# Kernel optimization log

Hardware: AMD Instinct MI355X
Metric: run time of the kernel (lower is better)

The kernel has to match this reference:

```python
import jax, jax.numpy as jnp
import numpy as np

N_NODES = 50000
N_EDGES = 200000
NODE_F = 64
EDGE_F = 16
HID = 32
LAT = 16


def _glorot(key, shape):
    fan_in, fan_out = shape[0], shape[1]
    lim = np.sqrt(6.0 / (fan_in + fan_out))
    return jax.random.uniform(key, shape, jnp.float32, -lim, lim)


def setup_inputs() -> dict:
    key = jax.random.key(0)
    ks = jax.random.split(key, 24)
    inp = {
        "x": jax.random.normal(ks[0], (N_NODES, NODE_F), jnp.float32),
        "edge_index": jax.random.randint(ks[1], (2, N_EDGES), 0, N_NODES, jnp.int64),
        "edge_attr": jax.random.normal(ks[2], (N_EDGES, EDGE_F), jnp.float32),
        # encoder input projection
        "lin_in_w": _glorot(ks[3], (NODE_F, HID)),
        "lin_in_b": jnp.zeros((HID,), jnp.float32),
        # 3 edge MLPs (stacked over layer axis)
        "edge_w1": jnp.stack([_glorot(ks[4 + i], (EDGE_F, HID)) for i in range(3)]),
        "edge_b1": jnp.zeros((3, HID), jnp.float32),
        "edge_w2": jnp.stack([_glorot(ks[7 + i], (HID, HID * HID)) * 0.1 for i in range(3)]),
        "edge_b2": jnp.zeros((3, HID * HID), jnp.float32),
        # 3 NNConv root weights + biases
        "root_w": jnp.stack([_glorot(ks[10 + i], (HID, HID)) for i in range(3)]),
        "root_b": jnp.zeros((3, HID), jnp.float32),
        # encoder output projection
        "lin_out_w": _glorot(ks[13], (HID, LAT)),
        "lin_out_b": jnp.zeros((LAT,), jnp.float32),
        # node decoder MLP
        "dec_w1": _glorot(ks[14], (LAT, HID)),
        "dec_b1": jnp.zeros((HID,), jnp.float32),
        "dec_w2": _glorot(ks[15], (HID, NODE_F)),
        "dec_b2": jnp.zeros((NODE_F,), jnp.float32),
    }
    return inp


def _nnconv(x, src, dst, edge_attr, w1, b1, w2, b2, root_w, root_b):
    # per-edge weight matrix from edge MLP: [E, H, H]
    h = jax.nn.relu(edge_attr @ w1 + b1)
    w_e = (h @ w2 + b2).reshape(-1, HID, HID)
    # gather source features, per-edge matmul: [E, H]
    msg = jnp.einsum("eh,eho->eo", x[src], w_e)
    # scatter-mean to destinations
    agg = jax.ops.segment_sum(msg, dst, num_segments=N_NODES)
    cnt = jax.ops.segment_sum(jnp.ones((msg.shape[0], 1), x.dtype), dst, num_segments=N_NODES)
    agg = agg / jnp.maximum(cnt, 1.0)
    # root weight + bias
    return agg + x @ root_w + root_b


def reference(x, edge_index, edge_attr, lin_in_w, lin_in_b, edge_w1, edge_b1,
              edge_w2, edge_b2, root_w, root_b, lin_out_w, lin_out_b,
              dec_w1, dec_b1, dec_w2, dec_b2):
    src, dst = edge_index[0], edge_index[1]
    h = jax.nn.relu(x @ lin_in_w + lin_in_b)
    for i in range(3):  # fixed number of conv layers (dropout is identity in eval)
        h = _nnconv(h, src, dst, edge_attr, edge_w1[i], edge_b1[i],
                    edge_w2[i], edge_b2[i], root_w[i], root_b[i])
        h = jax.nn.relu(h)
    z = h @ lin_out_w + lin_out_b
    # node decoder
    d = jax.nn.relu(z @ dec_w1 + dec_b1)
    return d @ dec_w2 + dec_b2
```

## Files before the change

kernel.cpp:

```cpp
#include <hip/hip_runtime.h>
#include <hip/hip_bf16.h>
#include <stdint.h>

#define N_NODES 50000
#define N_EDGES 200000
#define NODE_F 64
#define EDGE_F 16
#define HID 32
#define LAT 16
#define KTOT 1056
#define SCAN_BLOCKS 196

typedef __attribute__((ext_vector_type(8))) short short8;
typedef __attribute__((ext_vector_type(4))) float f32x4;
typedef __attribute__((ext_vector_type(2))) float f32x2;

static __device__ __forceinline__ unsigned short bfbits(float f) {
  union { __hip_bfloat16 h; unsigned short s; } c; c.h = __float2bfloat16(f); return c.s;
}
static __device__ __forceinline__ unsigned pk2(f32x2 v) {
  __hip_bfloat162 h = __float22bfloat162_rn(make_float2(v.x, v.y));
  unsigned u; __builtin_memcpy(&u, &h, 4); return u;
}
static __device__ __forceinline__ unsigned pkt(f32x2 v) {
  return __builtin_amdgcn_perm(__float_as_uint(v.y), __float_as_uint(v.x), 0x07060302u);
}
union AFrag { short8 v; unsigned u[4]; };

__global__ void k_prep(const float* __restrict__ ew2, const float* __restrict__ eb2,
                       const float* __restrict__ ew1,
                       unsigned short* __restrict__ w2t,
                       unsigned short* __restrict__ w1p,
                       int* __restrict__ deg) {
  int g = blockIdx.x*256 + threadIdx.x;
  int l = g / (HID*KTOT);
  int r = g % (HID*KTOT);
  int o = r / KTOT;
  int kg = r % KTOT;
  int k = kg >> 5, h = kg & 31;
  float v = (k < 32) ? ew2[(size_t)l*32768 + k*1024 + h*32 + o]
                     : eb2[(size_t)l*1024 + h*32 + o];
  w2t[g] = bfbits(v);
  if (g < N_NODES) deg[g] = 0;
  if (g < 3*2*64*8) {
    int l2 = g >> 10;
    int r2 = g & 1023;
    int nt = r2 >> 9;
    int ln = (r2 >> 3) & 63;
    int j  = r2 & 7;
    int kgr = ln >> 4;
    float w = (kgr < 2) ? ew1[(size_t)l2*512 + (kgr*8 + j)*32 + nt*16 + (ln & 15)] : 0.f;
    w1p[g] = bfbits(w);
  }
}

__global__ void k_hist(const int* __restrict__ ei, int* __restrict__ deg) {
  int t = blockIdx.x*256 + threadIdx.x;
  if (t >= N_EDGES) return;
  int d = ei[N_EDGES + t];
  d = min(max(d, 0), N_NODES-1);
  atomicAdd(&deg[d], 1);
}

__global__ __launch_bounds__(256) void k_scan1(const int* __restrict__ deg,
                                               int* __restrict__ off,
                                               int* __restrict__ bsum) {
  __shared__ int s[256];
  const int tid = threadIdx.x;
  const int t = blockIdx.x*256 + tid;
  int d = (t < N_NODES) ? deg[t] : 0;
  s[tid] = d; __syncthreads();
  int v = d;
  #pragma unroll
  for (int ofs = 1; ofs < 256; ofs <<= 1) {
    int w = (tid >= ofs) ? s[tid-ofs] : 0;
    __syncthreads();
    v += w; s[tid] = v;
    __syncthreads();
  }
  if (t < N_NODES) off[t] = v - d;
  if (tid == 255) bsum[blockIdx.x] = v;
}

__global__ __launch_bounds__(256) void k_scan2(int* __restrict__ bsum) {
  __shared__ int s[256];
  const int tid = threadIdx.x;
  int d = (tid < SCAN_BLOCKS) ? bsum[tid] : 0;
  s[tid] = d; __syncthreads();
  int v = d;
  #pragma unroll
  for (int ofs = 1; ofs < 256; ofs <<= 1) {
    int w = (tid >= ofs) ? s[tid-ofs] : 0;
    __syncthreads();
    v += w; s[tid] = v;
    __syncthreads();
  }
  if (tid < SCAN_BLOCKS) bsum[tid] = v - d;
}

__global__ void k_scan3(int* __restrict__ off, const int* __restrict__ bsum,
                        int* __restrict__ cursor) {
  int t = blockIdx.x*256 + threadIdx.x;
  if (t < N_NODES) {
    off[t] += bsum[t >> 8];
    cursor[t] = 0;
  }
  if (t == 0) off[N_NODES] = N_EDGES;
}

__global__ void k_scatter(const int* __restrict__ ei, const int* __restrict__ off,
                          int* __restrict__ cursor, int* __restrict__ elist) {
  int t = blockIdx.x*256 + threadIdx.x;
  if (t >= N_EDGES) return;
  int d = ei[N_EDGES + t];
  d = min(max(d, 0), N_NODES-1);
  int pos = atomicAdd(&cursor[d], 1);
  elist[off[d] + pos] = t;
}

__global__ void k_lin_in(const float* __restrict__ x,
                         const float* __restrict__ W,
                         const float* __restrict__ b,
                         float* __restrict__ h) {
  __shared__ float Ws[NODE_F*HID];
  __shared__ float bs[HID];
  for (int i = threadIdx.x; i < NODE_F*HID; i += 256) Ws[i] = W[i];
  if (threadIdx.x < HID) bs[threadIdx.x] = b[threadIdx.x];
  __syncthreads();
  int t = blockIdx.x*256 + threadIdx.x;
  if (t >= N_NODES*HID) return;
  int n = t >> 5, o = t & 31;
  const float4* xp = (const float4*)(x + (size_t)n*NODE_F);
  float acc = bs[o];
  #pragma unroll
  for (int j = 0; j < NODE_F/4; j++) {
    float4 v = xp[j];
    acc = fmaf(v.x, Ws[(4*j+0)*HID+o], acc);
    acc = fmaf(v.y, Ws[(4*j+1)*HID+o], acc);
    acc = fmaf(v.z, Ws[(4*j+2)*HID+o], acc);
    acc = fmaf(v.w, Ws[(4*j+3)*HID+o], acc);
  }
  h[t] = fmaxf(acc, 0.f);
}

__global__ __launch_bounds__(256) void k_msg(const float* __restrict__ hin,
                                             const float* __restrict__ ea,
                                             const int* __restrict__ ei,
                                             const unsigned short* __restrict__ w1pl,
                                             const float* __restrict__ b1,
                                             const unsigned short* __restrict__ w2tl,
                                             float* __restrict__ msg) {
  __shared__ float sHE[128*33];
  __shared__ int   sSRC[128];
  const int tid = threadIdx.x;
  const int be  = blockIdx.x*128;
  const int wv   = tid >> 6;
  const int lane = tid & 63;
  const int nn   = lane & 15;
  const int quad = lane >> 4;
  const int eb0  = wv*32;
  const int eb1  = wv*32 + 16;

  if (lane < 32) {
    int e = min(be + wv*32 + lane, N_EDGES-1);
    sSRC[wv*32 + lane] = min(max(ei[e], 0), N_NODES-1);
    sHE[(wv*32 + lane)*33 + 32] = 1.0f;
  }

  {
    AFrag a0, a1;
    if (quad < 2) {
      int e0 = min(be + eb0 + nn, N_EDGES-1);
      int e1 = min(be + eb1 + nn, N_EDGES-1);
      const float4* p0 = (const float4*)(ea + (size_t)e0*EDGE_F + quad*8);
      const float4* p1 = (const float4*)(ea + (size_t)e1*EDGE_F + quad*8);
      float4 u = p0[0], v = p0[1];
      float4 s = p1[0], t = p1[1];
      a0.u[0] = pkt(f32x2{u.x,u.y}); a0.u[1] = pkt(f32x2{u.z,u.w});
      a0.u[2] = pkt(f32x2{v.x,v.y}); a0.u[3] = pkt(f32x2{v.z,v.w});
      a1.u[0] = pkt(f32x2{s.x,s.y}); a1.u[1] = pkt(f32x2{s.z,s.w});
      a1.u[2] = pkt(f32x2{t.x,t.y}); a1.u[3] = pkt(f32x2{t.z,t.w});
    } else {
      #pragma unroll
      for (int i = 0; i < 4; i++) { a0.u[i] = 0u; a1.u[i] = 0u; }
    }
    short8 wb0 = *(const short8*)(w1pl + lane*8);
    short8 wb1 = *(const short8*)(w1pl + 512 + lane*8);
    f32x4 z = {0.f,0.f,0.f,0.f};
    f32x4 h00 = __builtin_amdgcn_mfma_f32_16x16x32_bf16(a0.v, wb0, z, 0, 0, 0);
    f32x4 h01 = __builtin_amdgcn_mfma_f32_16x16x32_bf16(a0.v, wb1, z, 0, 0, 0);
    f32x4 h10 = __builtin_amdgcn_mfma_f32_16x16x32_bf16(a1.v, wb0, z, 0, 0, 0);
    f32x4 h11 = __builtin_amdgcn_mfma_f32_16x16x32_bf16(a1.v, wb1, z, 0, 0, 0);
    float bv0 = b1[nn], bv1 = b1[nn + 16];
    #pragma unroll
    for (int r = 0; r < 4; r++) {
      int ro0 = (eb0 + quad*4 + r)*33;
      int ro1 = (eb1 + quad*4 + r)*33;
      sHE[ro0 + nn]      = fmaxf(h00[r] + bv0, 0.f);
      sHE[ro0 + 16 + nn] = fmaxf(h01[r] + bv1, 0.f);
      sHE[ro1 + nn]      = fmaxf(h10[r] + bv0, 0.f);
      sHE[ro1 + 16 + nn] = fmaxf(h11[r] + bv1, 0.f);
    }
  }

  f32x2 xA[4], xB[4];
  {
    int s0i = sSRC[eb0+nn];
    int s1i = sSRC[eb1+nn];
    const float4* p0 = (const float4*)(hin + (size_t)s0i*HID);
    const float4* p1 = (const float4*)(hin + (size_t)s1i*HID);
    float4 a0 = p0[quad*2], a1 = p0[quad*2+1];
    float4 b0 = p1[quad*2], b1v = p1[quad*2+1];
    xA[0] = f32x2{a0.x, a0.y}; xA[1] = f32x2{a0.z, a0.w};
    xA[2] = f32x2{a1.x, a1.y}; xA[3] = f32x2{a1.z, a1.w};
    xB[0] = f32x2{b0.x, b0.y}; xB[1] = f32x2{b0.z, b0.w};
    xB[2] = f32x2{b1v.x, b1v.y}; xB[3] = f32x2{b1v.z, b1v.w};
  }

  f32x4 c00 = {0.f,0.f,0.f,0.f}, c01 = c00, c10 = c00, c11 = c00;
  const unsigned short* bp0 = w2tl + (unsigned)nn*KTOT + quad*8;
  const unsigned short* bp1 = bp0 + 16*KTOT;
  const float* heRow0 = sHE + (eb0+nn)*33;
  const float* heRow1 = sHE + (eb1+nn)*33;

  short8 sb0[3], sb1[3];
  float  sh0[3], sh1[3];
  #pragma unroll
  for (int j = 0; j < 3; j++) {
    sb0[j] = *(const short8*)(bp0 + j*32);
    sb1[j] = *(const short8*)(bp1 + j*32);
    sh0[j] = heRow0[j];
    sh1[j] = heRow1[j];
  }

  #pragma unroll 1
  for (int base = 0; base < 30; base += 3) {
    #pragma unroll
    for (int j = 0; j < 3; j++) {
      const int kk = base + j;
      float hk0 = sh0[j], hk1 = sh1[j];
      AFrag a0, a1;
      #pragma unroll
      for (int i = 0; i < 4; i++) {
        a0.u[i] = pkt(xA[i]*hk0);
        a1.u[i] = pkt(xB[i]*hk1);
      }
      short8 cb0 = sb0[j], cb1 = sb1[j];
      c00 = __builtin_amdgcn_mfma_f32_16x16x32_bf16(a0.v, cb0, c00, 0, 0, 0);
      c01 = __builtin_amdgcn_mfma_f32_16x16x32_bf16(a0.v, cb1, c01, 0, 0, 0);
      c10 = __builtin_amdgcn_mfma_f32_16x16x32_bf16(a1.v, cb0, c10, 0, 0, 0);
      c11 = __builtin_amdgcn_mfma_f32_16x16x32_bf16(a1.v, cb1, c11, 0, 0, 0);
      sb0[j] = *(const short8*)(bp0 + (kk+3)*32);
      sb1[j] = *(const short8*)(bp1 + (kk+3)*32);
      sh0[j] = heRow0[kk+3];
      sh1[j] = heRow1[kk+3];
    }
  }
  #pragma unroll
  for (int j = 0; j < 3; j++) {
    float hk0 = sh0[j], hk1 = sh1[j];
    AFrag a0, a1;
    #pragma unroll
    for (int i = 0; i < 4; i++) {
      a0.u[i] = pkt(xA[i]*hk0);
      a1.u[i] = pkt(xB[i]*hk1);
    }
    c00 = __builtin_amdgcn_mfma_f32_16x16x32_bf16(a0.v, sb0[j], c00, 0, 0, 0);
    c01 = __builtin_amdgcn_mfma_f32_16x16x32_bf16(a0.v, sb1[j], c01, 0, 0, 0);
    c10 = __builtin_amdgcn_mfma_f32_16x16x32_bf16(a1.v, sb0[j], c10, 0, 0, 0);
    c11 = __builtin_amdgcn_mfma_f32_16x16x32_bf16(a1.v, sb1[j], c11, 0, 0, 0);
  }

  #pragma unroll
  for (int r = 0; r < 4; r++) {
    int e0 = be + eb0 + quad*4 + r;
    if (e0 < N_EDGES) {
      msg[(size_t)e0*HID +      nn] = c00[r];
      msg[(size_t)e0*HID + 16 + nn] = c01[r];
    }
    int e1 = be + eb1 + quad*4 + r;
    if (e1 < N_EDGES) {
      msg[(size_t)e1*HID +      nn] = c10[r];
      msg[(size_t)e1*HID + 16 + nn] = c11[r];
    }
  }
}

__global__ void k_gather(const float* __restrict__ msg,
                         const int* __restrict__ off, const int* __restrict__ elist,
                         const float* __restrict__ hin,
                         const float* __restrict__ rw,
                         const float* __restrict__ rb,
                         float* __restrict__ hout) {
  __shared__ float rws[HID*HID];
  __shared__ float rbs[HID];
  for (int i = threadIdx.x; i < HID*HID; i += 256) rws[i] = rw[i];
  if (threadIdx.x < HID) rbs[threadIdx.x] = rb[threadIdx.x];
  __syncthreads();
  int t = blockIdx.x*256 + threadIdx.x;
  if (t >= N_NODES*8) return;
  int n = t >> 3, oc = t & 7;
  int s0 = off[n], s1 = off[n+1];
  float a0 = 0.f, a1 = 0.f, a2 = 0.f, a3 = 0.f;
  for (int j = s0; j < s1; j++) {
    int e = elist[j];
    float4 v = ((const float4*)(msg + (size_t)e*HID))[oc];
    a0 += v.x; a1 += v.y; a2 += v.z; a3 += v.w;
  }
  float inv = 1.f / fmaxf((float)(s1 - s0), 1.f);
  a0 = fmaf(a0, inv, rbs[oc*4+0]);
  a1 = fmaf(a1, inv, rbs[oc*4+1]);
  a2 = fmaf(a2, inv, rbs[oc*4+2]);
  a3 = fmaf(a3, inv, rbs[oc*4+3]);
  const float4* hp = (const float4*)(hin + (size_t)n*HID);
  #pragma unroll
  for (int jq = 0; jq < 8; jq++) {
    float4 hv = hp[jq];
    #pragma unroll
    for (int c = 0; c < 4; c++) {
      int j = jq*4 + c;
      float h = (c==0)?hv.x:(c==1)?hv.y:(c==2)?hv.z:hv.w;
      const float4* rp = (const float4*)(rws + j*HID + oc*4);
      float4 r = rp[0];
      a0 = fmaf(h, r.x, a0);
      a1 = fmaf(h, r.y, a1);
      a2 = fmaf(h, r.z, a2);
      a3 = fmaf(h, r.w, a3);
    }
  }
  float4 res = make_float4(fmaxf(a0,0.f), fmaxf(a1,0.f), fmaxf(a2,0.f), fmaxf(a3,0.f));
  ((float4*)(hout + (size_t)n*HID))[oc] = res;
}

__global__ void k_decoder(const float* __restrict__ h,
                          const float* __restrict__ lo_w, const float* __restrict__ lo_b,
                          const float* __restrict__ d1_w, const float* __restrict__ d1_b,
                          const float* __restrict__ d2_w, const float* __restrict__ d2_b,
                          float* __restrict__ out) {
  __shared__ float lows[HID*LAT], lobs[LAT], d1s[LAT*HID], d1bs[HID], d2s[HID*NODE_F], d2bs[NODE_F];
  for (int i = threadIdx.x; i < HID*LAT; i += 256) lows[i] = lo_w[i];
  for (int i = threadIdx.x; i < LAT; i += 256) lobs[i] = lo_b[i];
  for (int i = threadIdx.x; i < LAT*HID; i += 256) d1s[i] = d1_w[i];
  for (int i = threadIdx.x; i < HID; i += 256) d1bs[i] = d1_b[i];
  for (int i = threadIdx.x; i < HID*NODE_F; i += 256) d2s[i] = d2_w[i];
  for (int i = threadIdx.x; i < NODE_F; i += 256) d2bs[i] = d2_b[i];
  __syncthreads();
  int n = blockIdx.x*256 + threadIdx.x;
  if (n >= N_NODES) return;
  float hr[HID];
  const float4* hp = (const float4*)(h + (size_t)n*HID);
  #pragma unroll
  for (int i = 0; i < HID/4; i++) { float4 v = hp[i]; hr[4*i]=v.x; hr[4*i+1]=v.y; hr[4*i+2]=v.z; hr[4*i+3]=v.w; }
  float z[LAT];
  #pragma unroll
  for (int o = 0; o < LAT; o++) {
    float a = lobs[o];
    #pragma unroll
    for (int j = 0; j < HID; j++) a = fmaf(hr[j], lows[j*LAT+o], a);
    z[o] = a;
  }
  float d[HID];
  #pragma unroll
  for (int o = 0; o < HID; o++) {
    float a = d1bs[o];
    #pragma unroll
    for (int j = 0; j < LAT; j++) a = fmaf(z[j], d1s[j*HID+o], a);
    d[o] = fmaxf(a, 0.f);
  }
  float* op = out + (size_t)n*NODE_F;
  #pragma unroll 8
  for (int o = 0; o < NODE_F; o++) {
    float a = d2bs[o];
    #pragma unroll
    for (int j = 0; j < HID; j++) a = fmaf(d[j], d2s[j*NODE_F+o], a);
    op[o] = a;
  }
}

extern "C" void kernel_launch(void* const* d_in, const int* in_sizes, int n_in,
                              void* d_out, int out_size, void* d_ws, size_t ws_size,
                              hipStream_t stream) {
  const float* x   = (const float*)d_in[0];
  const int*   ei  = (const int*)d_in[1];
  const float* ea  = (const float*)d_in[2];
  const float* liw = (const float*)d_in[3];
  const float* lib = (const float*)d_in[4];
  const float* ew1 = (const float*)d_in[5];
  const float* eb1 = (const float*)d_in[6];
  const float* ew2 = (const float*)d_in[7];
  const float* eb2 = (const float*)d_in[8];
  const float* rw  = (const float*)d_in[9];
  const float* rb  = (const float*)d_in[10];
  const float* low = (const float*)d_in[11];
  const float* lob = (const float*)d_in[12];
  const float* d1w = (const float*)d_in[13];
  const float* d1b = (const float*)d_in[14];
  const float* d2w = (const float*)d_in[15];
  const float* d2b = (const float*)d_in[16];
  float* out = (float*)d_out;

  float* h0   = (float*)d_ws;
  float* h1   = h0  + (size_t)N_NODES*HID;
  float* msg  = h1  + (size_t)N_NODES*HID;
  int*  deg   = (int*)(msg + (size_t)N_EDGES*HID);
  int*  off   = deg + N_NODES;
  int*  cursor= off + N_NODES + 16;
  int*  elist = cursor + N_NODES;
  int*  bsum  = elist + N_EDGES;
  unsigned short* w2t = (unsigned short*)(bsum + 256);
  unsigned short* w1p = w2t + 3*HID*KTOT;

  k_prep<<<(3*HID*KTOT)/256, 256, 0, stream>>>(ew2, eb2, ew1, w2t, w1p, deg);
  k_hist<<<(N_EDGES + 255)/256, 256, 0, stream>>>(ei, deg);
  k_scan1<<<SCAN_BLOCKS, 256, 0, stream>>>(deg, off, bsum);
  k_scan2<<<1, 256, 0, stream>>>(bsum);
  k_scan3<<<(N_NODES + 255)/256, 256, 0, stream>>>(off, bsum, cursor);
  k_scatter<<<(N_EDGES + 255)/256, 256, 0, stream>>>(ei, off, cursor, elist);

  k_lin_in<<<(N_NODES*HID + 255)/256, 256, 0, stream>>>(x, liw, lib, h0);

  float* hin = h0; float* hout = h1;
  for (int i = 0; i < 3; i++) {
    k_msg<<<(N_EDGES + 127)/128, 256, 0, stream>>>(hin, ea, ei,
        w1p + (size_t)i*1024, eb1 + i*HID,
        w2t + (size_t)i*HID*KTOT, msg);
    k_gather<<<(N_NODES*8 + 255)/256, 256, 0, stream>>>(msg, off, elist, hin,
        rw + i*HID*HID, rb + i*HID, hout);
    float* t = hin; hin = hout; hout = t;
  }

  k_decoder<<<(N_NODES + 255)/256, 256, 0, stream>>>(hin, low, lob, d1w, d1b, d2w, d2b, out);
}
```

Measured before the change: 321.4 us.

## Write messages in CSR order and process 64 edges per wave in k_msg

k_msg now handles 256 edges per block (four 16-edge tiles per wave), so each loaded W2 fragment is reused across four MFMA tiles instead of two. Messages are written straight to their CSR slot through a new per-edge position array filled by k_scatter. This lets k_gather read contiguous rows without the elist indirection. In exchange, k_msg's stores become scattered, register pressure rises with eight accumulators and sixteen x fragments, and there are half as many blocks.

```diff
diff --git a/kernel.cpp b/kernel.cpp
--- a/kernel.cpp
+++ b/kernel.cpp
@@ -17,10 +17,6 @@
 
 static __device__ __forceinline__ unsigned short bfbits(float f) {
   union { __hip_bfloat16 h; unsigned short s; } c; c.h = __float2bfloat16(f); return c.s;
-}
-static __device__ __forceinline__ unsigned pk2(f32x2 v) {
-  __hip_bfloat162 h = __float22bfloat162_rn(make_float2(v.x, v.y));
-  unsigned u; __builtin_memcpy(&u, &h, 4); return u;
 }
 static __device__ __forceinline__ unsigned pkt(f32x2 v) {
   return __builtin_amdgcn_perm(__float_as_uint(v.y), __float_as_uint(v.x), 0x07060302u);
@@ -109,13 +105,16 @@
 }
 
 __global__ void k_scatter(const int* __restrict__ ei, const int* __restrict__ off,
-                          int* __restrict__ cursor, int* __restrict__ elist) {
+                          int* __restrict__ cursor, int* __restrict__ elist,
+                          int* __restrict__ csr_pos) {
   int t = blockIdx.x*256 + threadIdx.x;
   if (t >= N_EDGES) return;
   int d = ei[N_EDGES + t];
   d = min(max(d, 0), N_NODES-1);
   int pos = atomicAdd(&cursor[d], 1);
-  elist[off[d] + pos] = t;
+  int slot = off[d] + pos;
+  elist[slot] = t;
+  csr_pos[t] = slot;
 }
 
 __global__ void k_lin_in(const float* __restrict__ x,
@@ -149,88 +148,84 @@
                                              const unsigned short* __restrict__ w1pl,
                                              const float* __restrict__ b1,
                                              const unsigned short* __restrict__ w2tl,
-                                             float* __restrict__ msg) {
-  __shared__ float sHE[128*33];
-  __shared__ int   sSRC[128];
+                                             const int* __restrict__ csr_pos,
+                                             float* __restrict__ msgS) {
+  __shared__ float sHE[256*33];
+  __shared__ int   sSRC[256];
+  __shared__ int   sPOS[256];
   const int tid = threadIdx.x;
-  const int be  = blockIdx.x*128;
+  const int be  = blockIdx.x*256;
   const int wv   = tid >> 6;
   const int lane = tid & 63;
   const int nn   = lane & 15;
   const int quad = lane >> 4;
-  const int eb0  = wv*32;
-  const int eb1  = wv*32 + 16;
-
-  if (lane < 32) {
-    int e = min(be + wv*32 + lane, N_EDGES-1);
-    sSRC[wv*32 + lane] = min(max(ei[e], 0), N_NODES-1);
-    sHE[(wv*32 + lane)*33 + 32] = 1.0f;
-  }
+  const int wbase = wv*64;
 
   {
-    AFrag a0, a1;
-    if (quad < 2) {
-      int e0 = min(be + eb0 + nn, N_EDGES-1);
-      int e1 = min(be + eb1 + nn, N_EDGES-1);
-      const float4* p0 = (const float4*)(ea + (size_t)e0*EDGE_F + quad*8);
-      const float4* p1 = (const float4*)(ea + (size_t)e1*EDGE_F + quad*8);
-      float4 u = p0[0], v = p0[1];
-      float4 s = p1[0], t = p1[1];
-      a0.u[0] = pkt(f32x2{u.x,u.y}); a0.u[1] = pkt(f32x2{u.z,u.w});
-      a0.u[2] = pkt(f32x2{v.x,v.y}); a0.u[3] = pkt(f32x2{v.z,v.w});
-      a1.u[0] = pkt(f32x2{s.x,s.y}); a1.u[1] = pkt(f32x2{s.z,s.w});
-      a1.u[2] = pkt(f32x2{t.x,t.y}); a1.u[3] = pkt(f32x2{t.z,t.w});
-    } else {
-      #pragma unroll
-      for (int i = 0; i < 4; i++) { a0.u[i] = 0u; a1.u[i] = 0u; }
-    }
+    int el = wbase + lane;
+    int e = min(be + el, N_EDGES-1);
+    sSRC[el] = min(max(ei[e], 0), N_NODES-1);
+    sPOS[el] = csr_pos[e];
+    sHE[el*33 + 32] = 1.0f;
+  }
+
+  {
     short8 wb0 = *(const short8*)(w1pl + lane*8);
     short8 wb1 = *(const short8*)(w1pl + 512 + lane*8);
     f32x4 z = {0.f,0.f,0.f,0.f};
-    f32x4 h00 = __builtin_amdgcn_mfma_f32_16x16x32_bf16(a0.v, wb0, z, 0, 0, 0);
-    f32x4 h01 = __builtin_amdgcn_mfma_f32_16x16x32_bf16(a0.v, wb1, z, 0, 0, 0);
-    f32x4 h10 = __builtin_amdgcn_mfma_f32_16x16x32_bf16(a1.v, wb0, z, 0, 0, 0);
-    f32x4 h11 = __builtin_amdgcn_mfma_f32_16x16x32_bf16(a1.v, wb1, z, 0, 0, 0);
     float bv0 = b1[nn], bv1 = b1[nn + 16];
     #pragma unroll
-    for (int r = 0; r < 4; r++) {
-      int ro0 = (eb0 + quad*4 + r)*33;
-      int ro1 = (eb1 + quad*4 + r)*33;
-      sHE[ro0 + nn]      = fmaxf(h00[r] + bv0, 0.f);
-      sHE[ro0 + 16 + nn] = fmaxf(h01[r] + bv1, 0.f);
-      sHE[ro1 + nn]      = fmaxf(h10[r] + bv0, 0.f);
-      sHE[ro1 + 16 + nn] = fmaxf(h11[r] + bv1, 0.f);
+    for (int t = 0; t < 4; t++) {
+      AFrag a;
+      if (quad < 2) {
+        int e = min(be + wbase + t*16 + nn, N_EDGES-1);
+        const float4* p = (const float4*)(ea + (size_t)e*EDGE_F + quad*8);
+        float4 u = p[0], v = p[1];
+        a.u[0] = pkt(f32x2{u.x,u.y}); a.u[1] = pkt(f32x2{u.z,u.w});
+        a.u[2] = pkt(f32x2{v.x,v.y}); a.u[3] = pkt(f32x2{v.z,v.w});
+      } else {
+        #pragma unroll
+        for (int i = 0; i < 4; i++) a.u[i] = 0u;
+      }
+      f32x4 h0 = __builtin_amdgcn_mfma_f32_16x16x32_bf16(a.v, wb0, z, 0, 0, 0);
+      f32x4 h1 = __builtin_amdgcn_mfma_f32_16x16x32_bf16(a.v, wb1, z, 0, 0, 0);
+      #pragma unroll
+      for (int r = 0; r < 4; r++) {
+        int ro = (wbase + t*16 + quad*4 + r)*33;
+        sHE[ro + nn]      = fmaxf(h0[r] + bv0, 0.f);
+        sHE[ro + 16 + nn] = fmaxf(h1[r] + bv1, 0.f);
+      }
     }
   }
 
-  f32x2 xA[4], xB[4];
-  {
-    int s0i = sSRC[eb0+nn];
-    int s1i = sSRC[eb1+nn];
-    const float4* p0 = (const float4*)(hin + (size_t)s0i*HID);
-    const float4* p1 = (const float4*)(hin + (size_t)s1i*HID);
-    float4 a0 = p0[quad*2], a1 = p0[quad*2+1];
-    float4 b0 = p1[quad*2], b1v = p1[quad*2+1];
-    xA[0] = f32x2{a0.x, a0.y}; xA[1] = f32x2{a0.z, a0.w};
-    xA[2] = f32x2{a1.x, a1.y}; xA[3] = f32x2{a1.z, a1.w};
-    xB[0] = f32x2{b0.x, b0.y}; xB[1] = f32x2{b0.z, b0.w};
-    xB[2] = f32x2{b1v.x, b1v.y}; xB[3] = f32x2{b1v.z, b1v.w};
-  }
-
-  f32x4 c00 = {0.f,0.f,0.f,0.f}, c01 = c00, c10 = c00, c11 = c00;
+  f32x2 xs[4][4];
+  #pragma unroll
+  for (int t = 0; t < 4; t++) {
+    int si = sSRC[wbase + t*16 + nn];
+    const float4* p = (const float4*)(hin + (size_t)si*HID);
+    float4 a = p[quad*2], b = p[quad*2+1];
+    xs[t][0] = f32x2{a.x, a.y}; xs[t][1] = f32x2{a.z, a.w};
+    xs[t][2] = f32x2{b.x, b.y}; xs[t][3] = f32x2{b.z, b.w};
+  }
+
+  f32x4 c0[4], c1[4];
+  #pragma unroll
+  for (int t = 0; t < 4; t++) { c0[t] = f32x4{0.f,0.f,0.f,0.f}; c1[t] = c0[t]; }
+
   const unsigned short* bp0 = w2tl + (unsigned)nn*KTOT + quad*8;
   const unsigned short* bp1 = bp0 + 16*KTOT;
-  const float* heRow0 = sHE + (eb0+nn)*33;
-  const float* heRow1 = sHE + (eb1+nn)*33;
+  const float* heR[4];
+  #pragma unroll
+  for (int t = 0; t < 4; t++) heR[t] = sHE + (wbase + t*16 + nn)*33;
 
   short8 sb0[3], sb1[3];
-  float  sh0[3], sh1[3];
+  float  sh[3][4];
   #pragma unroll
   for (int j = 0; j < 3; j++) {
     sb0[j] = *(const short8*)(bp0 + j*32);
     sb1[j] = *(const short8*)(bp1 + j*32);
-    sh0[j] = heRow0[j];
-    sh1[j] = heRow1[j];
+    #pragma unroll
+    for (int t = 0; t < 4; t++) sh[j][t] = heR[t][j];
   }
 
   #pragma unroll 1
@@ -238,56 +233,52 @@
     #pragma unroll
     for (int j = 0; j < 3; j++) {
       const int kk = base + j;
-      float hk0 = sh0[j], hk1 = sh1[j];
-      AFrag a0, a1;
+      short8 cb0 = sb0[j], cb1 = sb1[j];
       #pragma unroll
-      for (int i = 0; i < 4; i++) {
-        a0.u[i] = pkt(xA[i]*hk0);
-        a1.u[i] = pkt(xB[i]*hk1);
+      for (int t = 0; t < 4; t++) {
+        float hk = sh[j][t];
+        AFrag a;
+        #pragma unroll
+        for (int i = 0; i < 4; i++) a.u[i] = pkt(xs[t][i]*hk);
+        c0[t] = __builtin_amdgcn_mfma_f32_16x16x32_bf16(a.v, cb0, c0[t], 0, 0, 0);
+        c1[t] = __builtin_amdgcn_mfma_f32_16x16x32_bf16(a.v, cb1, c1[t], 0, 0, 0);
       }
-      short8 cb0 = sb0[j], cb1 = sb1[j];
-      c00 = __builtin_amdgcn_mfma_f32_16x16x32_bf16(a0.v, cb0, c00, 0, 0, 0);
-      c01 = __builtin_amdgcn_mfma_f32_16x16x32_bf16(a0.v, cb1, c01, 0, 0, 0);
-      c10 = __builtin_amdgcn_mfma_f32_16x16x32_bf16(a1.v, cb0, c10, 0, 0, 0);
-      c11 = __builtin_amdgcn_mfma_f32_16x16x32_bf16(a1.v, cb1, c11, 0, 0, 0);
       sb0[j] = *(const short8*)(bp0 + (kk+3)*32);
       sb1[j] = *(const short8*)(bp1 + (kk+3)*32);
-      sh0[j] = heRow0[kk+3];
-      sh1[j] = heRow1[kk+3];
+      #pragma unroll
+      for (int t = 0; t < 4; t++) sh[j][t] = heR[t][kk+3];
     }
   }
   #pragma unroll
   for (int j = 0; j < 3; j++) {
-    float hk0 = sh0[j], hk1 = sh1[j];
-    AFrag a0, a1;
-    #pragma unroll
-    for (int i = 0; i < 4; i++) {
-      a0.u[i] = pkt(xA[i]*hk0);
-      a1.u[i] = pkt(xB[i]*hk1);
+    short8 cb0 = sb0[j], cb1 = sb1[j];
+    #pragma unroll
+    for (int t = 0; t < 4; t++) {
+      float hk = sh[j][t];
+      AFrag a;
+      #pragma unroll
+      for (int i = 0; i < 4; i++) a.u[i] = pkt(xs[t][i]*hk);
+      c0[t] = __builtin_amdgcn_mfma_f32_16x16x32_bf16(a.v, cb0, c0[t], 0, 0, 0);
+      c1[t] = __builtin_amdgcn_mfma_f32_16x16x32_bf16(a.v, cb1, c1[t], 0, 0, 0);
     }
-    c00 = __builtin_amdgcn_mfma_f32_16x16x32_bf16(a0.v, sb0[j], c00, 0, 0, 0);
-    c01 = __builtin_amdgcn_mfma_f32_16x16x32_bf16(a0.v, sb1[j], c01, 0, 0, 0);
-    c10 = __builtin_amdgcn_mfma_f32_16x16x32_bf16(a1.v, sb0[j], c10, 0, 0, 0);
-    c11 = __builtin_amdgcn_mfma_f32_16x16x32_bf16(a1.v, sb1[j], c11, 0, 0, 0);
-  }
-
-  #pragma unroll
-  for (int r = 0; r < 4; r++) {
-    int e0 = be + eb0 + quad*4 + r;
-    if (e0 < N_EDGES) {
-      msg[(size_t)e0*HID +      nn] = c00[r];
-      msg[(size_t)e0*HID + 16 + nn] = c01[r];
+  }
+
+  #pragma unroll
+  for (int t = 0; t < 4; t++) {
+    #pragma unroll
+    for (int r = 0; r < 4; r++) {
+      int el = wbase + t*16 + quad*4 + r;
+      if (be + el < N_EDGES) {
+        size_t row = (size_t)sPOS[el]*HID;
+        msgS[row +      nn] = c0[t][r];
+        msgS[row + 16 + nn] = c1[t][r];
+      }
     }
-    int e1 = be + eb1 + quad*4 + r;
-    if (e1 < N_EDGES) {
-      msg[(size_t)e1*HID +      nn] = c10[r];
-      msg[(size_t)e1*HID + 16 + nn] = c11[r];
-    }
-  }
-}
-
-__global__ void k_gather(const float* __restrict__ msg,
-                         const int* __restrict__ off, const int* __restrict__ elist,
+  }
+}
+
+__global__ void k_gather(const float* __restrict__ msgS,
+                         const int* __restrict__ off,
                          const float* __restrict__ hin,
                          const float* __restrict__ rw,
                          const float* __restrict__ rb,
@@ -303,8 +294,7 @@
   int s0 = off[n], s1 = off[n+1];
   float a0 = 0.f, a1 = 0.f, a2 = 0.f, a3 = 0.f;
   for (int j = s0; j < s1; j++) {
-    int e = elist[j];
-    float4 v = ((const float4*)(msg + (size_t)e*HID))[oc];
+    float4 v = ((const float4*)(msgS + (size_t)j*HID))[oc];
     a0 += v.x; a1 += v.y; a2 += v.z; a3 += v.w;
   }
   float inv = 1.f / fmaxf((float)(s1 - s0), 1.f);
@@ -406,7 +396,8 @@
   int*  off   = deg + N_NODES;
   int*  cursor= off + N_NODES + 16;
   int*  elist = cursor + N_NODES;
-  int*  bsum  = elist + N_EDGES;
+  int*  cpos  = elist + N_EDGES;
+  int*  bsum  = cpos + N_EDGES;
   unsigned short* w2t = (unsigned short*)(bsum + 256);
   unsigned short* w1p = w2t + 3*HID*KTOT;
 
@@ -415,16 +406,16 @@
   k_scan1<<<SCAN_BLOCKS, 256, 0, stream>>>(deg, off, bsum);
   k_scan2<<<1, 256, 0, stream>>>(bsum);
   k_scan3<<<(N_NODES + 255)/256, 256, 0, stream>>>(off, bsum, cursor);
-  k_scatter<<<(N_EDGES + 255)/256, 256, 0, stream>>>(ei, off, cursor, elist);
+  k_scatter<<<(N_EDGES + 255)/256, 256, 0, stream>>>(ei, off, cursor, elist, cpos);
 
   k_lin_in<<<(N_NODES*HID + 255)/256, 256, 0, stream>>>(x, liw, lib, h0);
 
   float* hin = h0; float* hout = h1;
   for (int i = 0; i < 3; i++) {
-    k_msg<<<(N_EDGES + 127)/128, 256, 0, stream>>>(hin, ea, ei,
+    k_msg<<<(N_EDGES + 255)/256, 256, 0, stream>>>(hin, ea, ei,
         w1p + (size_t)i*1024, eb1 + i*HID,
-        w2t + (size_t)i*HID*KTOT, msg);
-    k_gather<<<(N_NODES*8 + 255)/256, 256, 0, stream>>>(msg, off, elist, hin,
+        w2t + (size_t)i*HID*KTOT, cpos, msg);
+    k_gather<<<(N_NODES*8 + 255)/256, 256, 0, stream>>>(msg, off, hin,
         rw + i*HID*HID, rb + i*HID, hout);
     float* t = hin; hin = hout; hout = t;
   }
```

Result: faster. 287.8 us (-10.5%).
